# Kernel optimization log

Measured on AMD Instinct MI355X. Metric: run time of the kernel, lower is better.

Reference implementation:

```python
import jax, jax.numpy as jnp
import numpy as np

# OFDM/MIMO constants from the source module
N = 512        # subcarriers
N_R = 2        # rx antennas
N_T = 2        # tx antennas
M_BITS = 4     # bits per QAM symbol (16-QAM)
CP = 7         # cyclic prefix = IsiDuration - 1
NO = 1e-5
EBNO_DB = 10.0
BATCH = 4096

# unit-average-power 16-QAM: per-axis levels, index = re_idx + 4*im_idx, bits LSB-first
LEV = jnp.asarray(np.array([-3.0, -1.0, 1.0, 3.0], np.float32) / np.sqrt(10.0))
_idx = np.arange(2 ** M_BITS)
CONST = jnp.asarray(((np.array([-3., -1., 1., 3.]) / np.sqrt(10.))[_idx % 4]
                     + 1j * (np.array([-3., -1., 1., 3.]) / np.sqrt(10.))[_idx // 4]).astype(np.complex64))


def setup_inputs() -> dict:
    key = jax.random.key(0)
    k1, k2, k3 = jax.random.split(key, 3)
    y_data_nld = jax.random.normal(k1, (BATCH, N_R, N + CP, 2), jnp.float32)
    y_ls = jax.random.normal(k2, (BATCH, N_R, N + CP, 2), jnp.float32)
    x_ls_idx = jax.random.randint(k3, (BATCH, N_T, N), 0, 2 ** M_BITS)
    return {"y_data_nld": y_data_nld, "y_ls": y_ls, "x_ls_idx": x_ls_idx}


def _c(x):
    return jax.lax.complex(x[..., 0], x[..., 1])


def _interp_c(xq, xp, fp):
    # fp: [M, P] complex -> [M, N] complex, linear interp per row (np.interp semantics)
    return jax.vmap(lambda fr, fi: jnp.interp(xq, xp, fr) + 1j * jnp.interp(xq, xp, fi))(fp.real, fp.imag)


def _forward(y_data_nld, y_ls, x_ls_idx):
    B = y_data_nld.shape[0]
    pi = 10.0 ** (EBNO_DB / 10.0) * NO * N          # = 0.0512
    sqrt_pi = jnp.sqrt(jnp.float32(pi))

    # strip CP, FFT, normalize (1/N * fft)
    Y = jnp.fft.fft(_c(y_data_nld)[..., CP:], axis=-1) / N            # [B, N_r, N]
    Y_l = jnp.fft.fft(_c(y_ls)[..., CP:], axis=-1) / (N * sqrt_pi)     # [B, N_r, N]

    x_ls = CONST[x_ls_idx]                                             # [B, N_t, N] pilots

    # comb-type LS estimates + linear interpolation to all N subcarriers
    xq = jnp.arange(N, dtype=jnp.float32)
    H_t = []
    for t in range(N_T):
        comb = jnp.arange(t, N, N_T)                                   # pilot subcarriers for tx t
        pil = Y_l[:, :, comb] / x_ls[:, None, t, comb]                 # [B, N_r, N/N_t]
        if t == 0:
            xp = jnp.concatenate([comb, jnp.array([N - 1])]).astype(jnp.float32)
            fp = jnp.concatenate([pil, pil[..., -1:]], axis=-1)
        else:
            xp = jnp.concatenate([jnp.array([0]), comb]).astype(jnp.float32)
            fp = jnp.concatenate([pil[..., :1], pil], axis=-1)
        P = fp.shape[-1]
        H_t.append(_interp_c(xq, xp, fp.reshape(B * N_R, P)).reshape(B, N_R, N))
    Hm = jnp.stack(H_t, axis=-1)                                       # [B, N_r, N, N_t]
    Hm = jnp.transpose(Hm, (0, 2, 1, 3))                               # [B, N, N_r, N_t]

    # per-subcarrier 2x2 linear solve: X_hat = H^{-1} Y / sqrt(pi)
    X_hat = jnp.linalg.solve(Hm, jnp.transpose(Y, (0, 2, 1))[..., None])[..., 0] / sqrt_pi  # [B, N, N_t]
    x_hat_ri = jnp.stack([X_hat.real, X_hat.imag], axis=-1)            # [B, N, N_t, 2]

    # nearest-QAM demap (square 16-QAM: per-axis argmin == joint argmin), bits LSB-first
    vre = jnp.argmin((X_hat.real[..., None] - LEV) ** 2, axis=-1)      # [B, N, N_t]
    vim = jnp.argmin((X_hat.imag[..., None] - LEV) ** 2, axis=-1)
    qidx = vre + 4 * vim
    bits = (qidx[..., None] >> jnp.arange(M_BITS)) & 1                 # [B, N, N_t, m]
    b_hat = jnp.transpose(bits, (0, 2, 1, 3)).reshape(B, N_T, N * M_BITS).astype(jnp.float32)
    return x_hat_ri, b_hat


def reference(y_data_nld, y_ls, x_ls_idx):
    return _forward(y_data_nld, y_ls, x_ls_idx)
```

## Files before the change

### kernel.cpp

```cpp
#include <hip/hip_runtime.h>

namespace {

constexpr int NSC  = 512;
constexpr int CP   = 7;
constexpr int NTOT = 519;

__device__ __forceinline__ int p2(int x) { return x + (x >> 4); }

struct cf { float x, y; };
__device__ __forceinline__ cf cadd(cf a, cf b) { return {a.x + b.x, a.y + b.y}; }
__device__ __forceinline__ cf csub(cf a, cf b) { return {a.x - b.x, a.y - b.y}; }
__device__ __forceinline__ cf cmul(cf a, cf b) { return {a.x*b.x - a.y*b.y, a.x*b.y + a.y*b.x}; }
__device__ __forceinline__ cf mni(cf a) { return {a.y, -a.x}; }

__device__ __forceinline__ void fft8(cf a[8]) {
    const float s = 0.70710678118654752f;
    cf b0 = a[0], b1 = a[4], b2 = a[2], b3 = a[6];
    cf b4 = a[1], b5 = a[5], b6 = a[3], b7 = a[7];
    cf c0 = cadd(b0, b1), c1 = csub(b0, b1);
    cf c2 = cadd(b2, b3), c3 = csub(b2, b3);
    cf c4 = cadd(b4, b5), c5 = csub(b4, b5);
    cf c6 = cadd(b6, b7), c7 = csub(b6, b7);
    cf d0 = cadd(c0, c2), d2 = csub(c0, c2);
    cf d1 = cadd(c1, mni(c3)), d3 = csub(c1, mni(c3));
    cf d4 = cadd(c4, c6), d6 = csub(c4, c6);
    cf d5 = cadd(c5, mni(c7)), d7 = csub(c5, mni(c7));
    cf e5 = { s * (d5.x + d5.y), s * (d5.y - d5.x) };
    cf e6 = mni(d6);
    cf e7 = { s * (d7.y - d7.x), -s * (d7.x + d7.y) };
    a[0] = cadd(d0, d4); a[4] = csub(d0, d4);
    a[1] = cadd(d1, e5); a[5] = csub(d1, e5);
    a[2] = cadd(d2, e6); a[6] = csub(d2, e6);
    a[3] = cadd(d3, e7); a[7] = csub(d3, e7);
}

struct cd { double x, y; };
__device__ __forceinline__ cd cmuld(cd a, cd b) { return {a.x*b.x - a.y*b.y, a.x*b.y + a.y*b.x}; }
__device__ __forceinline__ cd csubd(cd a, cd b) { return {a.x - b.x, a.y - b.y}; }

__global__ __launch_bounds__(256, 8) void ofdm_mimo_kernel(
    const float* __restrict__ y_data,
    const float* __restrict__ y_ls,
    const int*   __restrict__ x_idx,
    float*       __restrict__ out,
    int B)
{
    __shared__ cf sb[4][544];

    const int b   = blockIdx.x;
    const int tid = threadIdx.x;
    const int q   = tid >> 6;
    const int t   = tid & 63;

    const float sc = (float)(1.0 / (512.0 * 0.22627416997969522));

    const float W64A  = -6.2831853071795864769f / 64.0f;
    const float W512A = -6.2831853071795864769f / 512.0f;

    const int r = q & 1;
    const float* srcp = (q < 2) ? y_data : y_ls;
    const float2* xin = (const float2*)(srcp + ((size_t)(b * 2 + r) * NTOT + CP) * 2);

    cf a[8];
    #pragma unroll
    for (int n2 = 0; n2 < 8; ++n2) {
        float2 v = xin[t + 64 * n2];
        a[n2] = { v.x * sc, v.y * sc };
    }
    fft8(a);

    {
        const int n1 = t >> 3;
        float sn, cs;
        __sincosf(W64A * (float)n1, &sn, &cs);
        cf w1 = {cs, sn}, w = w1;
        #pragma unroll
        for (int k0 = 1; k0 < 8; ++k0) {
            a[k0] = cmul(a[k0], w);
            w = cmul(w, w1);
        }
    }
    #pragma unroll
    for (int k0 = 0; k0 < 8; ++k0) sb[q][p2(t * 8 + k0)] = a[k0];
    __builtin_amdgcn_wave_barrier();

    #pragma unroll
    for (int n1 = 0; n1 < 8; ++n1)
        a[n1] = sb[q][p2(n1 * 64 + (t & 7) * 8 + (t >> 3))];
    __builtin_amdgcn_wave_barrier();
    fft8(a);

    {
        const int n0 = t & 7, k0 = t >> 3;
        float sn, cs, sn2, cs2;
        __sincosf(W512A * (float)(n0 * k0), &sn, &cs);
        __sincosf(W64A * (float)n0, &sn2, &cs2);
        cf w = {cs, sn}, st = {cs2, sn2};
        #pragma unroll
        for (int k1 = 0; k1 < 8; ++k1) {
            a[k1] = cmul(a[k1], w);
            w = cmul(w, st);
        }
    }
    #pragma unroll
    for (int k1 = 0; k1 < 8; ++k1)
        sb[q][p2((t & 7) * 64 + (t >> 3) * 8 + k1)] = a[k1];
    __builtin_amdgcn_wave_barrier();

    #pragma unroll
    for (int n0 = 0; n0 < 8; ++n0)
        a[n0] = sb[q][p2(n0 * 64 + (t >> 3) * 8 + (t & 7))];
    __builtin_amdgcn_wave_barrier();
    fft8(a);

    #pragma unroll
    for (int k2 = 0; k2 < 8; ++k2)
        sb[q][p2((t >> 3) + 8 * (t & 7) + 64 * k2)] = a[k2];
    __syncthreads();

    const float lev[4] = {-0.9486832980505138f, -0.31622776601683794f,
                           0.31622776601683794f, 0.9486832980505138f};
    cf pv[2][2];
    #pragma unroll
    for (int j = 0; j < 2; ++j) {
        int u  = tid + 256 * j;
        int tt = u >> 8;
        int k  = u & 255;
        int comb = tt + 2 * k;
        int idx = x_idx[((size_t)(b * 2 + tt)) * NSC + comb];
        float xr = lev[idx & 3];
        float xi = lev[(idx >> 2) & 3];
        float inv = 1.0f / (xr * xr + xi * xi);
        #pragma unroll
        for (int rr = 0; rr < 2; ++rr) {
            cf yl = sb[2 + rr][p2(comb)];
            pv[j][rr] = { (yl.x * xr + yl.y * xi) * inv,
                          (yl.y * xr - yl.x * xi) * inv };
        }
    }
    __syncthreads();
    #pragma unroll
    for (int j = 0; j < 2; ++j) {
        int u  = tid + 256 * j;
        int tt = u >> 8;
        int k  = u & 255;
        #pragma unroll
        for (int rr = 0; rr < 2; ++rr)
            sb[2 + tt][p2(rr * 256 + k)] = pv[j][rr];
    }
    __syncthreads();

    #pragma unroll
    for (int ni = 0; ni < 2; ++ni) {
        const int n = tid + 256 * ni;
        const int kp = n >> 1;
        const int kR = (kp + 1 < 256) ? kp + 1 : 255;
        const int kL = (kp - 1 > 0) ? kp - 1 : 0;
        const float wA = (n & 1) ? 0.5f : 0.0f;
        const float wB = (n & 1) ? 0.0f : 0.5f;

        cd H[2][2];
        #pragma unroll
        for (int rr = 0; rr < 2; ++rr) {
            cf L0 = sb[2][p2(rr * 256 + kp)];
            cf R0 = sb[2][p2(rr * 256 + kR)];
            cf h0 = { L0.x + wA * (R0.x - L0.x), L0.y + wA * (R0.y - L0.y) };
            cf R1 = sb[3][p2(rr * 256 + kp)];
            cf L1 = sb[3][p2(rr * 256 + kL)];
            cf h1 = { R1.x + wB * (L1.x - R1.x), R1.y + wB * (L1.y - R1.y) };
            H[rr][0] = {(double)h0.x, (double)h0.y};
            H[rr][1] = {(double)h1.x, (double)h1.y};
        }
        cf y0 = sb[0][p2(n)], y1 = sb[1][p2(n)];
        cd Y0 = {(double)y0.x, (double)y0.y};
        cd Y1 = {(double)y1.x, (double)y1.y};

        cd det  = csubd(cmuld(H[0][0], H[1][1]), cmuld(H[0][1], H[1][0]));
        cd num0 = csubd(cmuld(H[1][1], Y0), cmuld(H[0][1], Y1));
        cd num1 = csubd(cmuld(H[0][0], Y1), cmuld(H[1][0], Y0));
        double invden = 1.0 / (det.x * det.x + det.y * det.y);
        cd X0 = { (num0.x * det.x + num0.y * det.y) * invden,
                  (num0.y * det.x - num0.x * det.y) * invden };
        cd X1 = { (num1.x * det.x + num1.y * det.y) * invden,
                  (num1.y * det.x - num1.x * det.y) * invden };

        float4* xo = (float4*)(out + (size_t)b * 2048 + (size_t)n * 4);
        *xo = make_float4((float)X0.x, (float)X0.y, (float)X1.x, (float)X1.y);

        const double bnd = 0.6324555320336759;
        auto qi = [&](double v) -> int {
            return (v <= -bnd) ? 0 : (v <= 0.0) ? 1 : (v <= bnd) ? 2 : 3;
        };
        int vre0 = qi(X0.x), vim0 = qi(X0.y);
        int vre1 = qi(X1.x), vim1 = qi(X1.y);

        size_t bbase = (size_t)B * 2048;
        float4* b0 = (float4*)(out + bbase + ((size_t)b * 2 + 0) * 2048 + (size_t)n * 4);
        *b0 = make_float4((float)(vre0 & 1), (float)((vre0 >> 1) & 1),
                          (float)(vim0 & 1), (float)((vim0 >> 1) & 1));
        float4* b1 = (float4*)(out + bbase + ((size_t)b * 2 + 1) * 2048 + (size_t)n * 4);
        *b1 = make_float4((float)(vre1 & 1), (float)((vre1 >> 1) & 1),
                          (float)(vim1 & 1), (float)((vim1 >> 1) & 1));
    }
}

}

extern "C" void kernel_launch(void* const* d_in, const int* in_sizes, int n_in,
                              void* d_out, int out_size, void* d_ws, size_t ws_size,
                              hipStream_t stream) {
    const float* y_data = (const float*)d_in[0];
    const float* y_ls   = (const float*)d_in[1];
    const int*   x_idx  = (const int*)d_in[2];
    float* out = (float*)d_out;

    int B = in_sizes[0] / (2 * NTOT * 2);
    ofdm_mimo_kernel<<<B, 256, 0, stream>>>(y_data, y_ls, x_idx, out, B);
}
```

Baseline: 35.27 us.

## Solve 2x2 in fp32, hoist pilot index loads, pack pilots as float4

Replaces the double-precision 2x2 complex solve and QAM decision with single-precision arithmetic. Moves the x_idx pilot loads and reciprocal computation ahead of the FFT so their latency overlaps it. Stores interpolated pilot estimates for both rx antennas as packed float4 in shared memory, so the interpolation stage needs fewer, wider LDS reads. Dropping fp64 removes slow double math on this GPU, but near-singular channels or symbols close to decision boundaries may now decode differently from the reference.

Result: faster. 33.79 us (-4.2%).

```diff
diff --git a/kernel.cpp b/kernel.cpp
--- a/kernel.cpp
+++ b/kernel.cpp
@@ -7,6 +7,7 @@
 constexpr int NTOT = 519;
 
 __device__ __forceinline__ int p2(int x) { return x + (x >> 4); }
+__device__ __forceinline__ int p4(int x) { return x + (x >> 4); }
 
 struct cf { float x, y; };
 __device__ __forceinline__ cf cadd(cf a, cf b) { return {a.x + b.x, a.y + b.y}; }
@@ -35,10 +36,6 @@
     a[3] = cadd(d3, e7); a[7] = csub(d3, e7);
 }
 
-struct cd { double x, y; };
-__device__ __forceinline__ cd cmuld(cd a, cd b) { return {a.x*b.x - a.y*b.y, a.x*b.y + a.y*b.x}; }
-__device__ __forceinline__ cd csubd(cd a, cd b) { return {a.x - b.x, a.y - b.y}; }
-
 __global__ __launch_bounds__(256, 8) void ofdm_mimo_kernel(
     const float* __restrict__ y_data,
     const float* __restrict__ y_ls,
@@ -57,6 +54,21 @@
 
     const float W64A  = -6.2831853071795864769f / 64.0f;
     const float W512A = -6.2831853071795864769f / 512.0f;
+
+    const float lev[4] = {-0.9486832980505138f, -0.31622776601683794f,
+                           0.31622776601683794f, 0.9486832980505138f};
+    float pxr[2], pxi[2], pinv[2];
+    #pragma unroll
+    for (int j = 0; j < 2; ++j) {
+        int u  = tid + 256 * j;
+        int k  = u & 255;
+        int comb = j + 2 * k;
+        int idx = x_idx[((size_t)(b * 2 + j)) * NSC + comb];
+        float xr = lev[idx & 3];
+        float xi = lev[(idx >> 2) & 3];
+        pxr[j] = xr; pxi[j] = xi;
+        pinv[j] = 1.0f / (xr * xr + xi * xi);
+    }
 
     const int r = q & 1;
     const float* srcp = (q < 2) ? y_data : y_ls;
@@ -119,38 +131,30 @@
         sb[q][p2((t >> 3) + 8 * (t & 7) + 64 * k2)] = a[k2];
     __syncthreads();
 
-    const float lev[4] = {-0.9486832980505138f, -0.31622776601683794f,
-                           0.31622776601683794f, 0.9486832980505138f};
-    cf pv[2][2];
+    float4 pout[2];
     #pragma unroll
     for (int j = 0; j < 2; ++j) {
-        int u  = tid + 256 * j;
-        int tt = u >> 8;
-        int k  = u & 255;
-        int comb = tt + 2 * k;
-        int idx = x_idx[((size_t)(b * 2 + tt)) * NSC + comb];
-        float xr = lev[idx & 3];
-        float xi = lev[(idx >> 2) & 3];
-        float inv = 1.0f / (xr * xr + xi * xi);
-        #pragma unroll
-        for (int rr = 0; rr < 2; ++rr) {
-            cf yl = sb[2 + rr][p2(comb)];
-            pv[j][rr] = { (yl.x * xr + yl.y * xi) * inv,
-                          (yl.y * xr - yl.x * xi) * inv };
-        }
+        int k  = (tid + 256 * j) & 255;
+        int comb = j + 2 * k;
+        cf y0l = sb[2][p2(comb)];
+        cf y1l = sb[3][p2(comb)];
+        pout[j] = make_float4((y0l.x * pxr[j] + y0l.y * pxi[j]) * pinv[j],
+                              (y0l.y * pxr[j] - y0l.x * pxi[j]) * pinv[j],
+                              (y1l.x * pxr[j] + y1l.y * pxi[j]) * pinv[j],
+                              (y1l.y * pxr[j] - y1l.x * pxi[j]) * pinv[j]);
     }
     __syncthreads();
-    #pragma unroll
-    for (int j = 0; j < 2; ++j) {
-        int u  = tid + 256 * j;
-        int tt = u >> 8;
-        int k  = u & 255;
-        #pragma unroll
-        for (int rr = 0; rr < 2; ++rr)
-            sb[2 + tt][p2(rr * 256 + k)] = pv[j][rr];
+    {
+        float4* pilA = (float4*)sb[2];
+        float4* pilB = (float4*)sb[3];
+        int k = tid & 255;
+        pilA[p4(k)] = pout[0];
+        pilB[p4(k)] = pout[1];
     }
     __syncthreads();
 
+    const float4* pilA = (const float4*)sb[2];
+    const float4* pilB = (const float4*)sb[3];
     #pragma unroll
     for (int ni = 0; ni < 2; ++ni) {
         const int n = tid + 256 * ni;
@@ -160,40 +164,37 @@
         const float wA = (n & 1) ? 0.5f : 0.0f;
         const float wB = (n & 1) ? 0.0f : 0.5f;
 
-        cd H[2][2];
-        #pragma unroll
-        for (int rr = 0; rr < 2; ++rr) {
-            cf L0 = sb[2][p2(rr * 256 + kp)];
-            cf R0 = sb[2][p2(rr * 256 + kR)];
-            cf h0 = { L0.x + wA * (R0.x - L0.x), L0.y + wA * (R0.y - L0.y) };
-            cf R1 = sb[3][p2(rr * 256 + kp)];
-            cf L1 = sb[3][p2(rr * 256 + kL)];
-            cf h1 = { R1.x + wB * (L1.x - R1.x), R1.y + wB * (L1.y - R1.y) };
-            H[rr][0] = {(double)h0.x, (double)h0.y};
-            H[rr][1] = {(double)h1.x, (double)h1.y};
-        }
-        cf y0 = sb[0][p2(n)], y1 = sb[1][p2(n)];
-        cd Y0 = {(double)y0.x, (double)y0.y};
-        cd Y1 = {(double)y1.x, (double)y1.y};
-
-        cd det  = csubd(cmuld(H[0][0], H[1][1]), cmuld(H[0][1], H[1][0]));
-        cd num0 = csubd(cmuld(H[1][1], Y0), cmuld(H[0][1], Y1));
-        cd num1 = csubd(cmuld(H[0][0], Y1), cmuld(H[1][0], Y0));
-        double invden = 1.0 / (det.x * det.x + det.y * det.y);
-        cd X0 = { (num0.x * det.x + num0.y * det.y) * invden,
-                  (num0.y * det.x - num0.x * det.y) * invden };
-        cd X1 = { (num1.x * det.x + num1.y * det.y) * invden,
-                  (num1.y * det.x - num1.x * det.y) * invden };
+        float4 L0 = pilA[p4(kp)];
+        float4 R0 = pilA[p4(kR)];
+        float4 R1 = pilB[p4(kp)];
+        float4 L1 = pilB[p4(kL)];
+
+        cf H00 = { L0.x + wA * (R0.x - L0.x), L0.y + wA * (R0.y - L0.y) };
+        cf H10 = { L0.z + wA * (R0.z - L0.z), L0.w + wA * (R0.w - L0.w) };
+        cf H01 = { R1.x + wB * (L1.x - R1.x), R1.y + wB * (L1.y - R1.y) };
+        cf H11 = { R1.z + wB * (L1.z - R1.z), R1.w + wB * (L1.w - R1.w) };
+
+        cf Y0 = sb[0][p2(n)];
+        cf Y1 = sb[1][p2(n)];
+
+        cf det  = csub(cmul(H00, H11), cmul(H01, H10));
+        cf num0 = csub(cmul(H11, Y0), cmul(H01, Y1));
+        cf num1 = csub(cmul(H00, Y1), cmul(H10, Y0));
+        float invden = 1.0f / (det.x * det.x + det.y * det.y);
+        float X0r = (num0.x * det.x + num0.y * det.y) * invden;
+        float X0i = (num0.y * det.x - num0.x * det.y) * invden;
+        float X1r = (num1.x * det.x + num1.y * det.y) * invden;
+        float X1i = (num1.y * det.x - num1.x * det.y) * invden;
 
         float4* xo = (float4*)(out + (size_t)b * 2048 + (size_t)n * 4);
-        *xo = make_float4((float)X0.x, (float)X0.y, (float)X1.x, (float)X1.y);
-
-        const double bnd = 0.6324555320336759;
-        auto qi = [&](double v) -> int {
-            return (v <= -bnd) ? 0 : (v <= 0.0) ? 1 : (v <= bnd) ? 2 : 3;
+        *xo = make_float4(X0r, X0i, X1r, X1i);
+
+        const float bnd = 0.63245553203367587f;
+        auto qi = [&](float v) -> int {
+            return (v <= -bnd) ? 0 : (v <= 0.0f) ? 1 : (v <= bnd) ? 2 : 3;
         };
-        int vre0 = qi(X0.x), vim0 = qi(X0.y);
-        int vre1 = qi(X1.x), vim1 = qi(X1.y);
+        int vre0 = qi(X0r), vim0 = qi(X0i);
+        int vre1 = qi(X1r), vim1 = qi(X1i);
 
         size_t bbase = (size_t)B * 2048;
         float4* b0 = (float4*)(out + bbase + ((size_t)b * 2 + 0) * 2048 + (size_t)n * 4);
```
